# Kernel tuning notes

Measured on AMD Instinct MI355X. Metric: run time of the kernel, lower is better.

Reference implementation:

```python
import jax, jax.numpy as jnp
import numpy as np

B, L, IN_DIM, D, H = 4, 1024, 256, 512, 8
DH = D // H
LARGE_NEG = -10000.0
LN_EPS = 1e-5


def _layernorm(x, g, b):
    mu = jnp.mean(x, axis=-1, keepdims=True)
    var = jnp.mean((x - mu) ** 2, axis=-1, keepdims=True)
    return (x - mu) * jax.lax.rsqrt(var + LN_EPS) * g + b


def setup_inputs() -> dict:
    key = jax.random.key(0)
    ks = jax.random.split(key, 16)
    s = 0.02
    return {
        "x": jax.random.normal(ks[0], (B, L, IN_DIM), jnp.float32),
        "attention_mask": jax.random.bernoulli(ks[1], 0.5, (B, L, L)),
        "adjacency_matrix": jax.random.uniform(ks[2], (B, L, L), jnp.float32),
        "W_fuse": jax.random.normal(ks[3], (D, IN_DIM), jnp.float32) * s,
        "b_fuse": jnp.zeros((D,), jnp.float32),
        "in_proj_w": jax.random.normal(ks[4], (3 * D, D), jnp.float32) * s,
        "in_proj_b": jnp.zeros((3 * D,), jnp.float32),
        "out_w": jax.random.normal(ks[5], (D, D), jnp.float32) * s,
        "out_b": jnp.zeros((D,), jnp.float32),
        "ln1_g": jnp.ones((D,), jnp.float32),
        "ln1_b": jnp.zeros((D,), jnp.float32),
        "ln2_g": jnp.ones((D,), jnp.float32),
        "ln2_b": jnp.zeros((D,), jnp.float32),
        "W1": jax.random.normal(ks[6], (4 * D, D), jnp.float32) * s,
        "b1": jnp.zeros((4 * D,), jnp.float32),
        "W2": jax.random.normal(ks[7], (D, 4 * D), jnp.float32) * s,
        "b2": jnp.zeros((D,), jnp.float32),
        "log_scale": jnp.array(0.0, jnp.float32),  # log(adj_bias_strength=1.0)
    }


def reference(x, attention_mask, adjacency_matrix, W_fuse, b_fuse, in_proj_w,
              in_proj_b, out_w, out_b, ln1_g, ln1_b, ln2_g, ln2_b,
              W1, b1, W2, b2, log_scale):
    # fuse projection (in_dim != d_model)
    x = jnp.einsum("bli,di->bld", x, W_fuse) + b_fuse

    # ensure_self_loops_in_mask: unmask diagonal of fully-masked rows
    eye = jnp.eye(L, dtype=bool)
    row_all = jnp.all(attention_mask, axis=-1)  # [B, L]
    mask = attention_mask & ~(eye[None, :, :] & row_all[:, :, None])

    # additive attention bias: large_neg where masked + scaled clipped adjacency
    bias = jnp.where(mask, LARGE_NEG, 0.0) + \
        jnp.exp(log_scale) * jnp.clip(adjacency_matrix, 0.0, 1.0)  # [B, L, L]

    # --- attention block (pre-norm) ---
    x_norm = _layernorm(x, ln1_g, ln1_b)
    qkv = jnp.einsum("bld,ed->ble", x_norm, in_proj_w) + in_proj_b
    q, k, v = jnp.split(qkv, 3, axis=-1)
    q = q.reshape(B, L, H, DH).transpose(0, 2, 1, 3)  # [B,H,L,DH]
    k = k.reshape(B, L, H, DH).transpose(0, 2, 1, 3)
    v = v.reshape(B, L, H, DH).transpose(0, 2, 1, 3)
    scores = jnp.einsum("bhqd,bhkd->bhqk", q, k) / np.sqrt(DH) + bias[:, None]
    probs = jax.nn.softmax(scores, axis=-1)
    ctx = jnp.einsum("bhqk,bhkd->bhqd", probs, v)
    ctx = ctx.transpose(0, 2, 1, 3).reshape(B, L, D)
    attn_out = jnp.einsum("bld,ed->ble", ctx, out_w) + out_b
    x = x + attn_out

    # --- FFN block (pre-norm) ---
    x_norm = _layernorm(x, ln2_g, ln2_b)
    h = jax.nn.gelu(jnp.einsum("bld,fd->blf", x_norm, W1) + b1, approximate=False)
    ff = jnp.einsum("blf,df->bld", h, W2) + b2
    return x + ff
```

## Files before the change

kernel.cpp:

```cpp
#include <hip/hip_runtime.h>
#include <math.h>

typedef unsigned short UST;
typedef __attribute__((ext_vector_type(8))) short bf16x8;
typedef __attribute__((ext_vector_type(4))) float f32x4;

#define BB 4
#define LL 1024
#define IND 256
#define DD 512
#define HH 8
#define FFD 2048
#define NT (BB*LL)

__device__ __forceinline__ float bf2f(UST u){ return __uint_as_float(((unsigned)u)<<16); }
__device__ __forceinline__ UST f2bf(float f){
  unsigned u = __float_as_uint(f);
  u += 0x7FFFu + ((u>>16)&1u);
  return (UST)(u>>16);
}
__device__ __forceinline__ float ldF(const void* p, long i, int isf32){
  return isf32 ? ((const float*)p)[i] : bf2f(((const UST*)p)[i]);
}
__device__ __forceinline__ bool ldMask(const void* p, long i, int fm){
  if (fm==0) return ((const int*)p)[i] != 0;
  if (fm==1) return ((const unsigned char*)p)[i] != 0;
  if (fm==2) return ((const UST*)p)[i] != 0;
  return ((const float*)p)[i] != 0.f;
}
__device__ __forceinline__ f32x4 mfma16(bf16x8 a, bf16x8 b, f32x4 c){
  return __builtin_amdgcn_mfma_f32_16x16x32_bf16(a, b, c, 0, 0, 0);
}
__device__ __forceinline__ void gld16(const void* g, void* l){
  __builtin_amdgcn_global_load_lds((const __attribute__((address_space(1))) unsigned int*)g,
                                   (__attribute__((address_space(3))) unsigned int*)l, 16, 0, 0);
}

__global__ void detect_k(int* flags, const UST* xh, const unsigned int* mw){
  int lane = threadIdx.x & 63;
  int e0 = (xh[lane] >> 7) & 0xFF;
  int e1 = (xh[64+lane] >> 7) & 0xFF;
  int f32 = __any((e0 >= 140) || (e1 >= 140)) ? 1 : 0;
  unsigned v = mw[lane];
  int w01   = __all(v <= 1u) ? 1 : 0;
  unsigned lo = v & 0xFFFFu, hi = v >> 16;
  int half  = __all((lo==0u||lo==0x3F80u) && (hi==0u||hi==0x3F80u)) ? 1 : 0;
  int wordF = __all(v==0u || v==0x3F800000u) ? 1 : 0;
  int byteB = __all((v & 0xFEFEFEFEu) == 0u) ? 1 : 0;
  if (lane == 0){
    flags[0] = f32;
    flags[1] = w01 ? 0 : (half ? (wordF ? 3 : 2) : (byteB ? 1 : 0));
  }
}

struct CvtArgs { const void* src[11]; UST* dst[11]; int n[11]; };
__global__ __launch_bounds__(256) void prep_k(const int* flags, CvtArgs a,
    const void* mask, const void* adj, const void* lsp, UST* biasOut){
  int bid = blockIdx.x;
  int t = threadIdx.x;
  if (bid < BB*LL){
    int fF = flags[0], fM = flags[1];
    int row = bid;
    int i = row & (LL-1);
    long base = (long)row * LL;
    int j0 = t*4;
    bool mv[4];
    if (fM == 0){
      int4 m4 = *(const int4*)((const int*)mask + base + j0);
      mv[0]=m4.x!=0; mv[1]=m4.y!=0; mv[2]=m4.z!=0; mv[3]=m4.w!=0;
    } else {
      #pragma unroll
      for (int k=0;k<4;++k) mv[k] = ldMask(mask, base + j0 + k, fM);
    }
    float a4[4];
    if (fF){
      float4 av = *(const float4*)((const float*)adj + base + j0);
      a4[0]=av.x; a4[1]=av.y; a4[2]=av.z; a4[3]=av.w;
    } else {
      const UST* ap = (const UST*)adj + base + j0;
      #pragma unroll
      for (int k=0;k<4;++k) a4[k] = bf2f(ap[k]);
    }
    int my = (mv[0]&&mv[1]&&mv[2]&&mv[3]) ? 1 : 0;
    int wa = __all(my);
    __shared__ int sAll[4];
    int w = t >> 6;
    if ((t & 63) == 0) sAll[w] = wa;
    __syncthreads();
    int rowAll = sAll[0] & sAll[1] & sAll[2] & sAll[3];
    float es = expf(ldF(lsp, 0, fF));
    UST o4[4];
    #pragma unroll
    for (int k = 0; k < 4; ++k){
      int j = j0 + k;
      float av = fminf(fmaxf(a4[k], 0.f), 1.f);
      bool eff = mv[k] && !((rowAll != 0) && (j == i));
      o4[k] = f2bf(((eff ? -10000.f : 0.f) + es * av) * 1.44269504f);
    }
    *(int2*)(biasOut + base + j0) = *(const int2*)o4;
  } else {
    int cb = bid - BB*LL;
    int ti = cb >> 9, xi = cb & 511;
    int n = a.n[ti];
    long i8 = ((long)xi*256 + t)*8;
    if (i8 >= n) return;
    const void* s = a.src[ti]; UST* d = a.dst[ti];
    if (flags[0]){
      const float4* sf = (const float4*)s;
      float4 a0 = sf[i8>>2], a1 = sf[(i8>>2)+1];
      UST o[8] = { f2bf(a0.x),f2bf(a0.y),f2bf(a0.z),f2bf(a0.w),
                   f2bf(a1.x),f2bf(a1.y),f2bf(a1.z),f2bf(a1.w) };
      *(int4*)(d+i8) = *(const int4*)o;
    } else {
      ((int4*)d)[i8>>3] = ((const int4*)s)[i8>>3];
    }
  }
}

template<int TM, int TN, int ACT, int RES, int OUTMODE>
__global__ __launch_bounds__(256) void gemm3_k(const int* flags,
    const UST* __restrict__ A, const UST* __restrict__ Bw, const UST* __restrict__ bias,
    const float* __restrict__ resid, void* Cout, int M, int N, int K, int Ks){
  constexpr int MI = TM/32, NI = TN/32;
  __shared__ UST sA[2][TM*64];
  __shared__ UST sB[2][TN*64];
  int t = threadIdx.x, w = t>>6, lane = t&63, l15 = lane&15, qd = lane>>4;
  int m0 = blockIdx.x*TM, n0 = blockIdx.y*TN;
  int zoff = blockIdx.z * Ks;
  int wm = (w&1)*(TM/2), wn = (w>>1)*(TN/2);
  f32x4 acc[MI][NI];
  #pragma unroll
  for (int mi=0; mi<MI; ++mi)
    #pragma unroll
    for (int ni=0; ni<NI; ++ni){ acc[mi][ni][0]=0;acc[mi][ni][1]=0;acc[mi][ni][2]=0;acc[mi][ni][3]=0; }
  int sRow = lane&7, sCol = (lane>>3)*8;
  const UST* aS = A + (long)(m0 + w*(TM/4) + sRow)*K + sCol + zoff;
  const UST* bS = Bw + (long)(n0 + w*(TN/4) + sRow)*K + sCol + zoff;
  auto stage = [&](int buf, int k0){
    #pragma unroll
    for (int c=0;c<MI;++c) gld16(aS + (long)c*8*K + k0, (char*)&sA[buf][(w*(TM/4)+c*8)*64]);
    #pragma unroll
    for (int c=0;c<NI;++c) gld16(bS + (long)c*8*K + k0, (char*)&sB[buf][(w*(TN/4)+c*8)*64]);
  };
  stage(0, 0);
  for (int k0 = 0; k0 < Ks; k0 += 64){
    int cur = (k0>>6)&1, nxt = cur^1;
    __syncthreads();
    if (k0 + 64 < Ks) stage(nxt, k0+64);
    #pragma unroll
    for (int ks=0; ks<2; ++ks){
      bf16x8 afr[MI], bfr[NI];
      #pragma unroll
      for (int mi=0; mi<MI; ++mi){
        int R = wm + mi*16 + l15;
        afr[mi] = *(const bf16x8*)&sA[cur][(R>>3)*512 + (ks*4+qd)*64 + (R&7)*8];
      }
      #pragma unroll
      for (int ni=0; ni<NI; ++ni){
        int R = wn + ni*16 + l15;
        bfr[ni] = *(const bf16x8*)&sB[cur][(R>>3)*512 + (ks*4+qd)*64 + (R&7)*8];
      }
      #pragma unroll
      for (int mi=0; mi<MI; ++mi)
        #pragma unroll
        for (int ni=0; ni<NI; ++ni)
          acc[mi][ni] = mfma16(afr[mi], bfr[ni], acc[mi][ni]);
    }
  }
  if (OUTMODE == 3){
    float* P = (float*)Cout + (size_t)blockIdx.z * M * N;
    #pragma unroll
    for (int mi=0; mi<MI; ++mi)
      #pragma unroll
      for (int ni=0; ni<NI; ++ni){
        int gc = n0 + wn + ni*16 + l15;
        #pragma unroll
        for (int r=0; r<4; ++r){
          int grow = m0 + wm + mi*16 + qd*4 + r;
          P[(long)grow*N + gc] = acc[mi][ni][r];
        }
      }
    return;
  }
  int outF32 = (OUTMODE==1) || (OUTMODE==2 && flags[0]);
  #pragma unroll
  for (int mi=0; mi<MI; ++mi){
    #pragma unroll
    for (int ni=0; ni<NI; ++ni){
      int gc = n0 + wn + ni*16 + l15;
      float bv = bf2f(bias[gc]);
      #pragma unroll
      for (int r=0; r<4; ++r){
        int grow = m0 + wm + mi*16 + qd*4 + r;
        float c = acc[mi][ni][r] + bv;
        if (ACT) c = 0.5f*c*(1.f+erff(c*0.70710678118654752f));
        long oi = (long)grow*N + gc;
        if (RES) c += resid[oi];
        if (outF32) ((float*)Cout)[oi] = c;
        else ((UST*)Cout)[oi] = f2bf(c);
      }
    }
  }
}

__global__ __launch_bounds__(256) void reduce4_k(const int* flags,
    const float* __restrict__ parts, const UST* __restrict__ bias,
    const float* __restrict__ resid, void* __restrict__ dout){
  const long S = (long)NT*DD;
  long e = ((long)blockIdx.x*256 + threadIdx.x)*4;
  float4 a = *(const float4*)(parts + e);
  float4 b = *(const float4*)(parts + S + e);
  float4 c = *(const float4*)(parts + 2*S + e);
  float4 d = *(const float4*)(parts + 3*S + e);
  float4 r = *(const float4*)(resid + e);
  int gc = (int)(e & (DD-1));
  float v[4] = { a.x+b.x+c.x+d.x + bf2f(bias[gc+0]) + r.x,
                 a.y+b.y+c.y+d.y + bf2f(bias[gc+1]) + r.y,
                 a.z+b.z+c.z+d.z + bf2f(bias[gc+2]) + r.z,
                 a.w+b.w+c.w+d.w + bf2f(bias[gc+3]) + r.w };
  if (flags[0]){
    *(float4*)((float*)dout + e) = *(const float4*)v;
  } else {
    UST o4[4] = { f2bf(v[0]), f2bf(v[1]), f2bf(v[2]), f2bf(v[3]) };
    *(int2*)((UST*)dout + e) = *(const int2*)o4;
  }
}

__global__ __launch_bounds__(256) void ln_k(const int* flags, const float* xin,
    const void* gp, const void* bp, UST* xout){
  int fF = flags[0];
  int row = blockIdx.x, t = threadIdx.x;
  const float* xr = xin + (long)row * DD;
  float v0 = xr[t], v1 = xr[t+256];
  float s = v0+v1, q = v0*v0 + v1*v1;
  #pragma unroll
  for (int off=1; off<64; off<<=1){ s += __shfl_xor(s,off,64); q += __shfl_xor(q,off,64); }
  __shared__ float rs[4], rq[4];
  int w = t>>6;
  if ((t&63)==0){ rs[w]=s; rq[w]=q; }
  __syncthreads();
  float S = rs[0]+rs[1]+rs[2]+rs[3];
  float Q = rq[0]+rq[1]+rq[2]+rq[3];
  float mean = S * (1.f/DD);
  float var  = fmaxf(Q * (1.f/DD) - mean*mean, 0.f);
  float ri = rsqrtf(var + 1e-5f);
  float g0 = ldF(gp, t, fF), b0 = ldF(bp, t, fF);
  float g1 = ldF(gp, t+256, fF), b1 = ldF(bp, t+256, fF);
  xout[(long)row*DD + t]     = f2bf((v0-mean)*ri*g0 + b0);
  xout[(long)row*DD + t+256] = f2bf((v1-mean)*ri*g1 + b1);
}

__global__ __launch_bounds__(256) void repack_v(const UST* __restrict__ qkv, UST* __restrict__ vT){
  int id = blockIdx.x;
  int bh = id & 31, qt = id >> 5;
  int b = bh >> 3, h = bh & 7;
  int t = threadIdx.x, w = t >> 6, lane = t & 63;
  int token = qt*64 + lane;
  const UST* src = qkv + ((long)(b*LL + token))*1536 + 1024 + h*64;
  #pragma unroll
  for (int c = 0; c < 2; ++c){
    int ch = w*2 + c;
    union { int4 v; UST u[8]; } uu;
    uu.v = *(const int4*)(src + ch*8);
    #pragma unroll
    for (int i = 0; i < 8; ++i)
      vT[((long)(bh*64 + ch*8 + i))*LL + token] = uu.u[i];
  }
}

__global__ __launch_bounds__(256) void attn_k(const UST* __restrict__ qkv,
    const UST* __restrict__ vT, const UST* __restrict__ bias, UST* __restrict__ ctx){
  int id = blockIdx.x;
  int b = id & 3, h = (id>>2) & 7, qt = id >> 5;
  int bh = b*HH + h;
  int q0 = qt*64;
  int t = threadIdx.x, w = t>>6, lane = t&63, l15 = lane&15, qd = lane>>4;
  __shared__ UST sK[2][2][64*32];
  __shared__ UST sV[2][2][64*32];
  __shared__ UST sB[2][2][64*32];
  __shared__ UST sP[4][16*72];
  UST* myP = &sP[w][0];

  const UST* qrow = qkv + ((long)(b*LL + q0 + w*16 + l15))*1536 + h*64;
  bf16x8 qf0 = *(const bf16x8*)(qrow + qd*8);
  bf16x8 qf1 = *(const bf16x8*)(qrow + 32 + qd*8);

  const UST* kS = qkv + (long)(b*LL + w*16 + (lane&15))*1536 + 512 + h*64 + (lane>>4)*8;
  const UST* vS = vT + (long)(bh*64 + w*16 + (lane&15))*LL + (lane>>4)*8;
  int rowS = t>>2, colS = (t&3)*8;
  const UST* bS = bias + ((long)b<<20) + (long)(q0 + rowS)*LL + colS;

  f32x4 o[4]; float lsum[4];
  #pragma unroll
  for (int i=0;i<4;i++){ o[i][0]=0;o[i][1]=0;o[i][2]=0;o[i][3]=0; lsum[i]=0.f; }
  const float C1 = 0.18033688f;

  auto stage = [&](int buf, int k0){
    gld16(kS + (long)k0*1536,      (char*)sK[buf][0] + w*1024);
    gld16(kS + (long)k0*1536 + 32, (char*)sK[buf][1] + w*1024);
    gld16(vS + k0,                 (char*)sV[buf][0] + w*1024);
    gld16(vS + k0 + 32,            (char*)sV[buf][1] + w*1024);
    gld16(bS + k0,                 (char*)sB[buf][0] + w*1024);
    gld16(bS + k0 + 32,            (char*)sB[buf][1] + w*1024);
  };
  stage(0, 0);

  for (int kt = 0; kt < 16; ++kt){
    int cur = kt&1, nxt = cur^1;
    int k0 = kt*64;
    __syncthreads();
    if (kt < 15) stage(nxt, k0+64);
    f32x4 s4[4];
    #pragma unroll
    for (int i=0;i<4;i++){ s4[i][0]=0;s4[i][1]=0;s4[i][2]=0;s4[i][3]=0; }
    #pragma unroll
    for (int ni=0; ni<4; ++ni){
      bf16x8 kf0 = *(const bf16x8*)&sK[cur][0][ni*512 + qd*128 + l15*8];
      bf16x8 kf1 = *(const bf16x8*)&sK[cur][1][ni*512 + qd*128 + l15*8];
      s4[ni] = mfma16(qf0, kf0, s4[ni]);
      s4[ni] = mfma16(qf1, kf1, s4[ni]);
    }
    float p[4][4];
    #pragma unroll
    for (int ni=0; ni<4; ++ni){
      const UST* sBc = sB[cur][ni>>1];
      int nc = (ni & 1)*16 + l15;
      #pragma unroll
      for (int r=0; r<4; ++r){
        float bzv = bf2f(sBc[(w*16 + qd*4 + r)*32 + nc]);
        p[ni][r] = exp2f(fmaf(s4[ni][r], C1, bzv));
      }
    }
    #pragma unroll
    for (int r=0; r<4; ++r)
      lsum[r] += (p[0][r]+p[1][r]) + (p[2][r]+p[3][r]);
    #pragma unroll
    for (int ni=0; ni<4; ++ni)
      #pragma unroll
      for (int r=0; r<4; ++r) myP[(qd*4+r)*72 + ni*16 + l15] = f2bf(p[ni][r]);
    bf16x8 pf0 = *(const bf16x8*)&myP[l15*72 + qd*8];
    bf16x8 pf1 = *(const bf16x8*)&myP[l15*72 + 32 + qd*8];
    #pragma unroll
    for (int dn=0; dn<4; ++dn){
      bf16x8 vf0 = *(const bf16x8*)&sV[cur][0][dn*512 + qd*128 + l15*8];
      bf16x8 vf1 = *(const bf16x8*)&sV[cur][1][dn*512 + qd*128 + l15*8];
      o[dn] = mfma16(pf0, vf0, o[dn]);
      o[dn] = mfma16(pf1, vf1, o[dn]);
    }
  }
  float linv[4];
  #pragma unroll
  for (int r=0; r<4; ++r){
    float s = lsum[r];
    #pragma unroll
    for (int off=1; off<16; off<<=1) s += __shfl_xor(s, off, 64);
    linv[r] = 1.f / s;
  }
  #pragma unroll
  for (int dn=0; dn<4; ++dn){
    #pragma unroll
    for (int r=0; r<4; ++r){
      long oi = ((long)(b*LL + q0 + w*16 + qd*4 + r))*DD + h*64 + dn*16 + l15;
      ctx[oi] = f2bf(o[dn][r] * linv[r]);
    }
  }
}

extern "C" void kernel_launch(void* const* d_in, const int* in_sizes, int n_in,
                              void* d_out, int out_size, void* d_ws, size_t ws_size,
                              hipStream_t stream){
  char* ws = (char*)d_ws;
  size_t o = 0;
  auto alloc = [&](size_t b){ size_t r = o; o += (b + 255) & ~(size_t)255; return r; };
  int*   flags = (int*)(ws + alloc(256));
  size_t biasOff = alloc(8UL<<20);
  size_t qkvOff  = alloc(12UL<<20);
  UST* biasC = (UST*)(ws + biasOff);
  UST* qkv   = (UST*)(ws + qkvOff);
  UST* hb    = (UST*)(ws + biasOff);
  UST* vT    = (UST*)(ws + alloc(4UL<<20));
  UST* xbf   = (UST*)(ws + alloc(2UL<<20));
  UST* wfuse = (UST*)(ws + alloc(131072*2));
  UST* bfuse = (UST*)(ws + alloc(1024));
  UST* ipw   = (UST*)(ws + alloc(786432*2));
  UST* ipb   = (UST*)(ws + alloc(3072*2));
  UST* outw  = (UST*)(ws + alloc(262144*2));
  UST* outb  = (UST*)(ws + alloc(1024));
  UST* w1    = (UST*)(ws + alloc(1048576*2));
  UST* b1    = (UST*)(ws + alloc(4096*2));
  UST* w2    = (UST*)(ws + alloc(1048576*2));
  UST* b2    = (UST*)(ws + alloc(1024));
  float* xf  = (float*)(ws + alloc((size_t)NT*DD*4));
  UST* xn    = (UST*)(ws + alloc((size_t)NT*DD*2));
  UST* ctx   = (UST*)(ws + alloc((size_t)NT*DD*2));
  float* x2  = (float*)(ws + alloc((size_t)NT*DD*4));
  size_t partsOff = alloc(4UL*NT*DD*4);
  float* parts = (float*)(ws + partsOff);
  bool doSplit = (o <= ws_size);

  detect_k<<<1, 64, 0, stream>>>(flags, (const UST*)d_in[0], (const unsigned int*)d_in[1]);

  CvtArgs ca;
  const int srcIdx[11] = {0,3,4,5,6,7,8,13,14,15,16};
  UST* dsts[11] = {xbf,wfuse,bfuse,ipw,ipb,outw,outb,w1,b1,w2,b2};
  const int ns[11] = {NT*IND, DD*IND, DD, 3*DD*DD, 3*DD, DD*DD, DD, FFD*DD, FFD, DD*FFD, DD};
  for (int i=0;i<11;i++){ ca.src[i]=d_in[srcIdx[i]]; ca.dst[i]=dsts[i]; ca.n[i]=ns[i]; }
  prep_k<<<BB*LL + 11*512, 256, 0, stream>>>(flags, ca, d_in[1], d_in[2], d_in[17], biasC);

  gemm3_k<64,64,0,0,1><<<dim3(64,8), 256, 0, stream>>>(flags, xbf, wfuse, bfuse, nullptr, xf, NT, DD, IND, IND);
  ln_k<<<NT, 256, 0, stream>>>(flags, xf, d_in[9], d_in[10], xn);
  gemm3_k<64,128,0,0,0><<<dim3(64,12), 256, 0, stream>>>(flags, xn, ipw, ipb, nullptr, qkv, NT, 3*DD, DD, DD);
  repack_v<<<512, 256, 0, stream>>>(qkv, vT);
  attn_k<<<512, 256, 0, stream>>>(qkv, vT, biasC, ctx);
  gemm3_k<64,64,0,1,1><<<dim3(64,8), 256, 0, stream>>>(flags, ctx, outw, outb, xf, x2, NT, DD, DD, DD);
  ln_k<<<NT, 256, 0, stream>>>(flags, x2, d_in[11], d_in[12], xn);
  gemm3_k<128,128,1,0,0><<<dim3(32,16), 256, 0, stream>>>(flags, xn, w1, b1, nullptr, hb, NT, FFD, DD, DD);
  if (doSplit){
    gemm3_k<128,128,0,0,3><<<dim3(32,4,4), 256, 0, stream>>>(flags, hb, w2, b2, nullptr, parts, NT, DD, FFD, FFD/4);
    reduce4_k<<<(NT*DD)/1024, 256, 0, stream>>>(flags, parts, b2, x2, d_out);
  } else {
    gemm3_k<64,64,0,1,2><<<dim3(64,8), 256, 0, stream>>>(flags, hb, w2, b2, x2, d_out, NT, DD, FFD, FFD);
  }
}
```

Baseline: 263.4 us.

## Split attention over key halves and pre-tile bias into MFMA fragment layout

```diff
diff --git a/kernel.cpp b/kernel.cpp
--- a/kernel.cpp
+++ b/kernel.cpp
@@ -58,6 +58,8 @@
     const void* mask, const void* adj, const void* lsp, UST* biasOut){
   int bid = blockIdx.x;
   int t = threadIdx.x;
+  __shared__ UST sTile[1024];
+  __shared__ int sAll[4];
   if (bid < BB*LL){
     int fF = flags[0], fM = flags[1];
     int row = bid;
@@ -83,7 +85,6 @@
     }
     int my = (mv[0]&&mv[1]&&mv[2]&&mv[3]) ? 1 : 0;
     int wa = __all(my);
-    __shared__ int sAll[4];
     int w = t >> 6;
     if ((t & 63) == 0) sAll[w] = wa;
     __syncthreads();
@@ -97,7 +98,17 @@
       bool eff = mv[k] && !((rowAll != 0) && (j == i));
       o4[k] = f2bf(((eff ? -10000.f : 0.f) + es * av) * 1.44269504f);
     }
-    *(int2*)(biasOut + base + j0) = *(const int2*)o4;
+    *(int2*)&sTile[j0] = *(const int2*)o4;
+    __syncthreads();
+    int kt = t >> 4, l15 = t & 15;
+    UST g4[4];
+    #pragma unroll
+    for (int ni=0; ni<4; ++ni) g4[ni] = sTile[kt*64 + ni*16 + l15];
+    int b = row >> 10, rr = row & 1023;
+    int qt = rr >> 6, q = rr & 63;
+    int w2 = q >> 4, qd = (q >> 2) & 3, r = q & 3;
+    long dst = ((long)((b*16 + qt)*16 + kt))*4096 + w2*1024 + (qd*16 + l15)*16 + r*4;
+    *(int2*)(biasOut + dst) = *(const int2*)g4;
   } else {
     int cb = bid - BB*LL;
     int ti = cb >> 9, xi = cb & 511;
@@ -269,15 +280,15 @@
 }
 
 __global__ __launch_bounds__(256) void attn_k(const UST* __restrict__ qkv,
-    const UST* __restrict__ vT, const UST* __restrict__ bias, UST* __restrict__ ctx){
+    const UST* __restrict__ vT, const UST* __restrict__ bias2,
+    float* __restrict__ oPart, float* __restrict__ lsumPart){
   int id = blockIdx.x;
-  int b = id & 3, h = (id>>2) & 7, qt = id >> 5;
+  int b = id & 3, h = (id>>2) & 7, slice = (id>>5) & 1, qt = id >> 6;
   int bh = b*HH + h;
   int q0 = qt*64;
   int t = threadIdx.x, w = t>>6, lane = t&63, l15 = lane&15, qd = lane>>4;
   __shared__ UST sK[2][2][64*32];
   __shared__ UST sV[2][2][64*32];
-  __shared__ UST sB[2][2][64*32];
   __shared__ UST sP[4][16*72];
   UST* myP = &sP[w][0];
 
@@ -287,8 +298,7 @@
 
   const UST* kS = qkv + (long)(b*LL + w*16 + (lane&15))*1536 + 512 + h*64 + (lane>>4)*8;
   const UST* vS = vT + (long)(bh*64 + w*16 + (lane&15))*LL + (lane>>4)*8;
-  int rowS = t>>2, colS = (t&3)*8;
-  const UST* bS = bias + ((long)b<<20) + (long)(q0 + rowS)*LL + colS;
+  const UST* bP = bias2 + ((long)((b*16 + qt)*16))*4096 + w*1024 + lane*16;
 
   f32x4 o[4]; float lsum[4];
   #pragma unroll
@@ -300,16 +310,20 @@
     gld16(kS + (long)k0*1536 + 32, (char*)sK[buf][1] + w*1024);
     gld16(vS + k0,                 (char*)sV[buf][0] + w*1024);
     gld16(vS + k0 + 32,            (char*)sV[buf][1] + w*1024);
-    gld16(bS + k0,                 (char*)sB[buf][0] + w*1024);
-    gld16(bS + k0 + 32,            (char*)sB[buf][1] + w*1024);
   };
-  stage(0, 0);
-
-  for (int kt = 0; kt < 16; ++kt){
+  int ktBase = slice*8;
+  stage(0, ktBase*64);
+  int4 bc0 = *(const int4*)(bP + (long)ktBase*4096);
+  int4 bc1 = *(const int4*)(bP + (long)ktBase*4096 + 8);
+
+  for (int kt = 0; kt < 8; ++kt){
     int cur = kt&1, nxt = cur^1;
-    int k0 = kt*64;
+    int k0 = (ktBase + kt)*64;
     __syncthreads();
-    if (kt < 15) stage(nxt, k0+64);
+    if (kt < 7) stage(nxt, k0+64);
+    int kn = ktBase + (kt < 7 ? kt+1 : 7);
+    int4 bn0 = *(const int4*)(bP + (long)kn*4096);
+    int4 bn1 = *(const int4*)(bP + (long)kn*4096 + 8);
     f32x4 s4[4];
     #pragma unroll
     for (int i=0;i<4;i++){ s4[i][0]=0;s4[i][1]=0;s4[i][2]=0;s4[i][3]=0; }
@@ -320,17 +334,18 @@
       s4[ni] = mfma16(qf0, kf0, s4[ni]);
       s4[ni] = mfma16(qf1, kf1, s4[ni]);
     }
+    union { int4 v; UST u[8]; } B0, B1;
+    B0.v = bc0; B1.v = bc1;
     float p[4][4];
     #pragma unroll
     for (int ni=0; ni<4; ++ni){
-      const UST* sBc = sB[cur][ni>>1];
-      int nc = (ni & 1)*16 + l15;
       #pragma unroll
       for (int r=0; r<4; ++r){
-        float bzv = bf2f(sBc[(w*16 + qd*4 + r)*32 + nc]);
-        p[ni][r] = exp2f(fmaf(s4[ni][r], C1, bzv));
+        UST bu = (r < 2) ? B0.u[r*4 + ni] : B1.u[(r&1)*4 + ni];
+        p[ni][r] = exp2f(fmaf(s4[ni][r], C1, bf2f(bu)));
       }
     }
+    bc0 = bn0; bc1 = bn1;
     #pragma unroll
     for (int r=0; r<4; ++r)
       lsum[r] += (p[0][r]+p[1][r]) + (p[2][r]+p[3][r]);
@@ -348,22 +363,41 @@
       o[dn] = mfma16(pf1, vf1, o[dn]);
     }
   }
-  float linv[4];
+  long lsBase = ((long)(slice*32 + bh))*LL + q0 + w*16;
   #pragma unroll
   for (int r=0; r<4; ++r){
     float s = lsum[r];
     #pragma unroll
     for (int off=1; off<16; off<<=1) s += __shfl_xor(s, off, 64);
-    linv[r] = 1.f / s;
-  }
+    if (l15 == r) lsumPart[lsBase + qd*4 + r] = s;
+  }
+  float* oDst = oPart + (size_t)slice * NT * DD;
   #pragma unroll
   for (int dn=0; dn<4; ++dn){
     #pragma unroll
     for (int r=0; r<4; ++r){
       long oi = ((long)(b*LL + q0 + w*16 + qd*4 + r))*DD + h*64 + dn*16 + l15;
-      ctx[oi] = f2bf(o[dn][r] * linv[r]);
-    }
-  }
+      oDst[oi] = o[dn][r];
+    }
+  }
+}
+
+__global__ __launch_bounds__(256) void combine_k(const float* __restrict__ oPart,
+    const float* __restrict__ lsumPart, UST* __restrict__ ctx){
+  const long S = (long)NT*DD;
+  long e = ((long)blockIdx.x*256 + threadIdx.x)*4;
+  float4 a = *(const float4*)(oPart + e);
+  float4 c = *(const float4*)(oPart + S + e);
+  long row = e >> 9;
+  int col = (int)(e & (DD-1));
+  int b = (int)(row >> 10), tok = (int)(row & 1023), h = col >> 6;
+  int bh = b*HH + h;
+  float l0 = lsumPart[(long)bh*LL + tok];
+  float l1 = lsumPart[(long)(32 + bh)*LL + tok];
+  float rinv = 1.f / (l0 + l1);
+  UST o4[4] = { f2bf((a.x+c.x)*rinv), f2bf((a.y+c.y)*rinv),
+                f2bf((a.z+c.z)*rinv), f2bf((a.w+c.w)*rinv) };
+  *(int2*)(ctx + e) = *(const int2*)o4;
 }
 
 extern "C" void kernel_launch(void* const* d_in, const int* in_sizes, int n_in,
@@ -394,6 +428,8 @@
   UST* xn    = (UST*)(ws + alloc((size_t)NT*DD*2));
   UST* ctx   = (UST*)(ws + alloc((size_t)NT*DD*2));
   float* x2  = (float*)(ws + alloc((size_t)NT*DD*4));
+  float* oPart = (float*)(ws + alloc(2UL*NT*DD*4));
+  float* lsumP = (float*)(ws + alloc(2UL*32*LL*4));
   size_t partsOff = alloc(4UL*NT*DD*4);
   float* parts = (float*)(ws + partsOff);
   bool doSplit = (o <= ws_size);
@@ -411,7 +447,8 @@
   ln_k<<<NT, 256, 0, stream>>>(flags, xf, d_in[9], d_in[10], xn);
   gemm3_k<64,128,0,0,0><<<dim3(64,12), 256, 0, stream>>>(flags, xn, ipw, ipb, nullptr, qkv, NT, 3*DD, DD, DD);
   repack_v<<<512, 256, 0, stream>>>(qkv, vT);
-  attn_k<<<512, 256, 0, stream>>>(qkv, vT, biasC, ctx);
+  attn_k<<<1024, 256, 0, stream>>>(qkv, vT, biasC, oPart, lsumP);
+  combine_k<<<(NT*DD)/1024, 256, 0, stream>>>(oPart, lsumP, ctx);
   gemm3_k<64,64,0,1,1><<<dim3(64,8), 256, 0, stream>>>(flags, ctx, outw, outb, xf, x2, NT, DD, DD, DD);
   ln_k<<<NT, 256, 0, stream>>>(flags, x2, d_in[11], d_in[12], xn);
   gemm3_k<128,128,1,0,0><<<dim3(32,16), 256, 0, stream>>>(flags, xn, w1, b1, nullptr, hb, NT, FFD, DD, DD);
```

Measured after the change: 269.2 us. +2.2%, slower.

## Pre-swizzle attention bias into MFMA fragment layout and fold detect into prep

Applied to the files above, without the earlier changes.

```diff
diff --git a/kernel.cpp b/kernel.cpp
--- a/kernel.cpp
+++ b/kernel.cpp
@@ -36,30 +36,34 @@
                                    (__attribute__((address_space(3))) unsigned int*)l, 16, 0, 0);
 }
 
-__global__ void detect_k(int* flags, const UST* xh, const unsigned int* mw){
-  int lane = threadIdx.x & 63;
-  int e0 = (xh[lane] >> 7) & 0xFF;
-  int e1 = (xh[64+lane] >> 7) & 0xFF;
-  int f32 = __any((e0 >= 140) || (e1 >= 140)) ? 1 : 0;
-  unsigned v = mw[lane];
-  int w01   = __all(v <= 1u) ? 1 : 0;
-  unsigned lo = v & 0xFFFFu, hi = v >> 16;
-  int half  = __all((lo==0u||lo==0x3F80u) && (hi==0u||hi==0x3F80u)) ? 1 : 0;
-  int wordF = __all(v==0u || v==0x3F800000u) ? 1 : 0;
-  int byteB = __all((v & 0xFEFEFEFEu) == 0u) ? 1 : 0;
-  if (lane == 0){
-    flags[0] = f32;
-    flags[1] = w01 ? 0 : (half ? (wordF ? 3 : 2) : (byteB ? 1 : 0));
-  }
-}
-
 struct CvtArgs { const void* src[11]; UST* dst[11]; int n[11]; };
-__global__ __launch_bounds__(256) void prep_k(const int* flags, CvtArgs a,
-    const void* mask, const void* adj, const void* lsp, UST* biasOut){
+__global__ __launch_bounds__(256) void prep_k(int* flags, CvtArgs a,
+    const UST* xh, const void* mask, const void* adj, const void* lsp, UST* biasOut){
   int bid = blockIdx.x;
   int t = threadIdx.x;
+  __shared__ UST sTile[1024];
+  __shared__ int sAll[4];
+  __shared__ int sFlags[2];
+  if (t < 64){
+    int lane = t;
+    int e0 = (xh[lane] >> 7) & 0xFF;
+    int e1 = (xh[64+lane] >> 7) & 0xFF;
+    int f32 = __any((e0 >= 140) || (e1 >= 140)) ? 1 : 0;
+    unsigned v = ((const unsigned int*)mask)[lane];
+    int w01   = __all(v <= 1u) ? 1 : 0;
+    unsigned lo = v & 0xFFFFu, hi = v >> 16;
+    int half  = __all((lo==0u||lo==0x3F80u) && (hi==0u||hi==0x3F80u)) ? 1 : 0;
+    int wordF = __all(v==0u || v==0x3F800000u) ? 1 : 0;
+    int byteB = __all((v & 0xFEFEFEFEu) == 0u) ? 1 : 0;
+    if (lane == 0){
+      int fm = w01 ? 0 : (half ? (wordF ? 3 : 2) : (byteB ? 1 : 0));
+      sFlags[0] = f32; sFlags[1] = fm;
+      if (bid == 0){ flags[0] = f32; flags[1] = fm; }
+    }
+  }
+  __syncthreads();
+  int fF = sFlags[0], fM = sFlags[1];
   if (bid < BB*LL){
-    int fF = flags[0], fM = flags[1];
     int row = bid;
     int i = row & (LL-1);
     long base = (long)row * LL;
@@ -83,7 +87,6 @@
     }
     int my = (mv[0]&&mv[1]&&mv[2]&&mv[3]) ? 1 : 0;
     int wa = __all(my);
-    __shared__ int sAll[4];
     int w = t >> 6;
     if ((t & 63) == 0) sAll[w] = wa;
     __syncthreads();
@@ -97,7 +100,17 @@
       bool eff = mv[k] && !((rowAll != 0) && (j == i));
       o4[k] = f2bf(((eff ? -10000.f : 0.f) + es * av) * 1.44269504f);
     }
-    *(int2*)(biasOut + base + j0) = *(const int2*)o4;
+    *(int2*)&sTile[j0] = *(const int2*)o4;
+    __syncthreads();
+    int kt = t >> 4, l15 = t & 15;
+    UST g4[4];
+    #pragma unroll
+    for (int ni=0; ni<4; ++ni) g4[ni] = sTile[kt*64 + ni*16 + l15];
+    int b = row >> 10, rr = row & 1023;
+    int qt = rr >> 6, q = rr & 63;
+    int w2 = q >> 4, qd = (q >> 2) & 3, r = q & 3;
+    long dst = ((long)((b*16 + qt)*16 + kt))*4096 + w2*1024 + (qd*16 + l15)*16 + r*4;
+    *(int2*)(biasOut + dst) = *(const int2*)g4;
   } else {
     int cb = bid - BB*LL;
     int ti = cb >> 9, xi = cb & 511;
@@ -105,7 +118,7 @@
     long i8 = ((long)xi*256 + t)*8;
     if (i8 >= n) return;
     const void* s = a.src[ti]; UST* d = a.dst[ti];
-    if (flags[0]){
+    if (fF){
       const float4* sf = (const float4*)s;
       float4 a0 = sf[i8>>2], a1 = sf[(i8>>2)+1];
       UST o[8] = { f2bf(a0.x),f2bf(a0.y),f2bf(a0.z),f2bf(a0.w),
@@ -269,7 +282,7 @@
 }
 
 __global__ __launch_bounds__(256) void attn_k(const UST* __restrict__ qkv,
-    const UST* __restrict__ vT, const UST* __restrict__ bias, UST* __restrict__ ctx){
+    const UST* __restrict__ vT, const UST* __restrict__ bias2, UST* __restrict__ ctx){
   int id = blockIdx.x;
   int b = id & 3, h = (id>>2) & 7, qt = id >> 5;
   int bh = b*HH + h;
@@ -277,7 +290,6 @@
   int t = threadIdx.x, w = t>>6, lane = t&63, l15 = lane&15, qd = lane>>4;
   __shared__ UST sK[2][2][64*32];
   __shared__ UST sV[2][2][64*32];
-  __shared__ UST sB[2][2][64*32];
   __shared__ UST sP[4][16*72];
   UST* myP = &sP[w][0];
 
@@ -287,8 +299,7 @@
 
   const UST* kS = qkv + (long)(b*LL + w*16 + (lane&15))*1536 + 512 + h*64 + (lane>>4)*8;
   const UST* vS = vT + (long)(bh*64 + w*16 + (lane&15))*LL + (lane>>4)*8;
-  int rowS = t>>2, colS = (t&3)*8;
-  const UST* bS = bias + ((long)b<<20) + (long)(q0 + rowS)*LL + colS;
+  const UST* bP = bias2 + ((long)((b*16 + qt)*16))*4096 + w*1024 + lane*16;
 
   f32x4 o[4]; float lsum[4];
   #pragma unroll
@@ -300,16 +311,19 @@
     gld16(kS + (long)k0*1536 + 32, (char*)sK[buf][1] + w*1024);
     gld16(vS + k0,                 (char*)sV[buf][0] + w*1024);
     gld16(vS + k0 + 32,            (char*)sV[buf][1] + w*1024);
-    gld16(bS + k0,                 (char*)sB[buf][0] + w*1024);
-    gld16(bS + k0 + 32,            (char*)sB[buf][1] + w*1024);
   };
   stage(0, 0);
+  int4 bc0 = *(const int4*)(bP);
+  int4 bc1 = *(const int4*)(bP + 8);
 
   for (int kt = 0; kt < 16; ++kt){
     int cur = kt&1, nxt = cur^1;
     int k0 = kt*64;
     __syncthreads();
     if (kt < 15) stage(nxt, k0+64);
+    int kn = (kt < 15 ? kt+1 : 15);
+    int4 bn0 = *(const int4*)(bP + (long)kn*4096);
+    int4 bn1 = *(const int4*)(bP + (long)kn*4096 + 8);
     f32x4 s4[4];
     #pragma unroll
     for (int i=0;i<4;i++){ s4[i][0]=0;s4[i][1]=0;s4[i][2]=0;s4[i][3]=0; }
@@ -320,17 +334,18 @@
       s4[ni] = mfma16(qf0, kf0, s4[ni]);
       s4[ni] = mfma16(qf1, kf1, s4[ni]);
     }
+    union { int4 v; UST u[8]; } B0, B1;
+    B0.v = bc0; B1.v = bc1;
     float p[4][4];
     #pragma unroll
     for (int ni=0; ni<4; ++ni){
-      const UST* sBc = sB[cur][ni>>1];
-      int nc = (ni & 1)*16 + l15;
       #pragma unroll
       for (int r=0; r<4; ++r){
-        float bzv = bf2f(sBc[(w*16 + qd*4 + r)*32 + nc]);
-        p[ni][r] = exp2f(fmaf(s4[ni][r], C1, bzv));
+        UST bu = (r < 2) ? B0.u[r*4 + ni] : B1.u[(r&1)*4 + ni];
+        p[ni][r] = exp2f(fmaf(s4[ni][r], C1, bf2f(bu)));
       }
     }
+    bc0 = bn0; bc1 = bn1;
     #pragma unroll
     for (int r=0; r<4; ++r)
       lsum[r] += (p[0][r]+p[1][r]) + (p[2][r]+p[3][r]);
@@ -398,14 +413,13 @@
   float* parts = (float*)(ws + partsOff);
   bool doSplit = (o <= ws_size);
 
-  detect_k<<<1, 64, 0, stream>>>(flags, (const UST*)d_in[0], (const unsigned int*)d_in[1]);
-
   CvtArgs ca;
   const int srcIdx[11] = {0,3,4,5,6,7,8,13,14,15,16};
   UST* dsts[11] = {xbf,wfuse,bfuse,ipw,ipb,outw,outb,w1,b1,w2,b2};
   const int ns[11] = {NT*IND, DD*IND, DD, 3*DD*DD, 3*DD, DD*DD, DD, FFD*DD, FFD, DD*FFD, DD};
   for (int i=0;i<11;i++){ ca.src[i]=d_in[srcIdx[i]]; ca.dst[i]=dsts[i]; ca.n[i]=ns[i]; }
-  prep_k<<<BB*LL + 11*512, 256, 0, stream>>>(flags, ca, d_in[1], d_in[2], d_in[17], biasC);
+  prep_k<<<BB*LL + 11*512, 256, 0, stream>>>(flags, ca, (const UST*)d_in[0],
+                                             d_in[1], d_in[2], d_in[17], biasC);
 
   gemm3_k<64,64,0,0,1><<<dim3(64,8), 256, 0, stream>>>(flags, xbf, wfuse, bfuse, nullptr, xf, NT, DD, IND, IND);
   ln_k<<<NT, 256, 0, stream>>>(flags, xf, d_in[9], d_in[10], xn);
```

After: 262.3 us. About the same (-0.4%).
